# Kernel optimization log

Measured on AMD Instinct MI355X. Metric: run time of the kernel, lower is better.

The kernel has to match this reference:

```python
import jax, jax.numpy as jnp
import numpy as np

N = 50000      # nodes
E = 800000     # edges (before self-loops)
IN = 128       # in_channels
H = 4          # heads
F = 32         # out_channels per head
NEG_SLOPE = 0.2  # GATConv default negative_slope


def setup_inputs() -> dict:
    key = jax.random.key(0)
    k1, k2, k3, k4, k5 = jax.random.split(key, 5)
    x = jax.random.normal(k1, (N, IN), dtype=jnp.float32)
    edge_index = jax.random.randint(k2, (2, E), 0, N, dtype=jnp.int32)
    W = jax.random.normal(k3, (IN, H * F), dtype=jnp.float32) * 0.05
    att_src = jax.random.normal(k4, (H, F), dtype=jnp.float32) * 0.05
    att_dst = jax.random.normal(k5, (H, F), dtype=jnp.float32) * 0.05
    bias = jnp.zeros((H * F,), dtype=jnp.float32)
    return {"x": x, "edge_index": edge_index, "W": W,
            "att_src": att_src, "att_dst": att_dst, "bias": bias}


def reference(x, edge_index, W, att_src, att_dst, bias):
    n = x.shape[0]
    # Linear projection, split into heads: [N, H, F]
    xp = (x @ W).reshape(n, H, F)
    # add_self_loops=True (GATConv default)
    loop = jnp.arange(n, dtype=edge_index.dtype)
    src = jnp.concatenate([edge_index[0], loop])  # [E+N]
    dst = jnp.concatenate([edge_index[1], loop])  # [E+N]
    # Per-node attention logits: [N, H]
    a_s = jnp.einsum('nhf,hf->nh', xp, att_src)
    a_d = jnp.einsum('nhf,hf->nh', xp, att_dst)
    # Edge logits + LeakyReLU: [E+N, H]
    e = jax.nn.leaky_relu(a_s[src] + a_d[dst], NEG_SLOPE)
    # Segment softmax over incoming edges of each dst node
    m = jax.ops.segment_max(e, dst, num_segments=n)  # every node has a self-loop
    e = jnp.exp(e - m[dst])
    denom = jax.ops.segment_sum(e, dst, num_segments=n)
    alpha = e / denom[dst]                     # [E+N, H]
    # Weighted aggregation of source features: [N, H, F]
    msg = alpha[:, :, None] * xp[src]
    out = jax.ops.segment_sum(msg, dst, num_segments=n)
    out = out.reshape(n, H * F) + bias         # concat heads + bias
    return jax.nn.relu(out)                    # wrapper activation (dropout = eval identity)
```

## Files before the change

kernel.cpp:

```cpp
#include <hip/hip_runtime.h>

#define HEADS 4
#define BSHIFT 8

__device__ __forceinline__ unsigned pack_bf16x2(float a, float b) {
  unsigned ua = __builtin_bit_cast(unsigned, a);
  unsigned ub = __builtin_bit_cast(unsigned, b);
  ua = (ua + 0x7FFFu + ((ua >> 16) & 1u)) >> 16;
  ub = (ub + 0x7FFFu + ((ub >> 16) & 1u)) >> 16;
  return ua | (ub << 16);
}
__device__ __forceinline__ float bf_lo(unsigned u) {
  return __builtin_bit_cast(float, u << 16);
}
__device__ __forceinline__ float bf_hi(unsigned u) {
  return __builtin_bit_cast(float, u & 0xFFFF0000u);
}

__global__ __launch_bounds__(256, 4) void k_gemm(
    const float* __restrict__ x, const float* __restrict__ W,
    const float* __restrict__ att_src, const float* __restrict__ att_dst,
    unsigned* __restrict__ xpb, float* __restrict__ a_s, float* __restrict__ a_d, int n)
{
  __shared__ float Wl[32 * 128];
  __shared__ float xs[64 * 36];
  const int tid = threadIdx.x;
  const int row0 = blockIdx.x * 64;
  const int rg = tid & 15;
  const int cg = tid >> 4;

  float acc[4][8];
#pragma unroll
  for (int i = 0; i < 4; ++i)
#pragma unroll
    for (int j = 0; j < 8; ++j) acc[i][j] = 0.f;

  for (int k0 = 0; k0 < 128; k0 += 32) {
    for (int i = tid; i < 1024; i += 256)
      ((float4*)Wl)[i] = ((const float4*)W)[(size_t)k0 * 32 + i];
    for (int i = tid; i < 512; i += 256) {
      const int r = i >> 3, kq = i & 7;
      float4 v = make_float4(0.f, 0.f, 0.f, 0.f);
      if (row0 + r < n) v = ((const float4*)x)[(size_t)(row0 + r) * 32 + (k0 >> 2) + kq];
      *(float4*)&xs[r * 36 + kq * 4] = v;
    }
    __syncthreads();

#pragma unroll
    for (int kk = 0; kk < 32; kk += 4) {
      float4 xr[4];
#pragma unroll
      for (int i = 0; i < 4; ++i) xr[i] = *(const float4*)&xs[(rg + 16 * i) * 36 + kk];
#pragma unroll
      for (int k = 0; k < 4; ++k) {
        float4 w0 = *(const float4*)&Wl[(kk + k) * 128 + 8 * cg];
        float4 w1 = *(const float4*)&Wl[(kk + k) * 128 + 8 * cg + 4];
        const float wv[8] = {w0.x, w0.y, w0.z, w0.w, w1.x, w1.y, w1.z, w1.w};
#pragma unroll
        for (int i = 0; i < 4; ++i) {
          const float xv = (k == 0) ? xr[i].x : (k == 1) ? xr[i].y : (k == 2) ? xr[i].z : xr[i].w;
#pragma unroll
          for (int j = 0; j < 8; ++j) acc[i][j] += xv * wv[j];
        }
      }
    }
    __syncthreads();
  }

  float4 as0 = ((const float4*)att_src)[2 * cg], as1 = ((const float4*)att_src)[2 * cg + 1];
  float4 ad0 = ((const float4*)att_dst)[2 * cg], ad1 = ((const float4*)att_dst)[2 * cg + 1];
  const float asv[8] = {as0.x, as0.y, as0.z, as0.w, as1.x, as1.y, as1.z, as1.w};
  const float adv[8] = {ad0.x, ad0.y, ad0.z, ad0.w, ad1.x, ad1.y, ad1.z, ad1.w};
  const int h = cg >> 2;

#pragma unroll
  for (int i = 0; i < 4; ++i) {
    const int r = row0 + rg + 16 * i;
    if (r < n) {
      uint4 ob;
      ob.x = pack_bf16x2(acc[i][0], acc[i][1]);
      ob.y = pack_bf16x2(acc[i][2], acc[i][3]);
      ob.z = pack_bf16x2(acc[i][4], acc[i][5]);
      ob.w = pack_bf16x2(acc[i][6], acc[i][7]);
      ((uint4*)xpb)[(size_t)r * 16 + cg] = ob;
    }
    float ps = 0.f, pd = 0.f;
#pragma unroll
    for (int j = 0; j < 8; ++j) { ps += acc[i][j] * asv[j]; pd += acc[i][j] * adv[j]; }
    ps += __shfl_xor(ps, 16); pd += __shfl_xor(pd, 16);
    ps += __shfl_xor(ps, 32); pd += __shfl_xor(pd, 32);
    if (r < n && (cg & 3) == 0) {
      a_s[r * HEADS + h] = ps;
      a_d[r * HEADS + h] = pd;
    }
  }
}

__global__ __launch_bounds__(256) void k_hist(
    const int* __restrict__ dst, int* __restrict__ ghist, int E)
{
  __shared__ int h[256];
  const int t = threadIdx.x;
  h[t] = 0;
  __syncthreads();
  int i = blockIdx.x * 1024 + t;
#pragma unroll
  for (int k = 0; k < 4; ++k, i += 256)
    if (i < E) atomicAdd(&h[dst[i] >> BSHIFT], 1);
  __syncthreads();
  if (h[t]) atomicAdd(&ghist[t], h[t]);
}

__global__ __launch_bounds__(256) void k_bscan(
    const int* __restrict__ ghist, int* __restrict__ gstart, int* __restrict__ gcur)
{
  __shared__ int wsum[4];
  const int t = threadIdx.x, lane = t & 63, w = t >> 6;
  const int v = ghist[t];
  int s = v;
#pragma unroll
  for (int o = 1; o < 64; o <<= 1) { int u = __shfl_up(s, o); if (lane >= o) s += u; }
  if (lane == 63) wsum[w] = s;
  __syncthreads();
  int add = 0;
  for (int k = 0; k < w; ++k) add += wsum[k];
  const int excl = add + s - v;
  gstart[t] = excl;
  gcur[t] = excl;
  if (t == 255) gstart[256] = excl + v;
}

__global__ __launch_bounds__(256) void k_part(
    const int* __restrict__ src, const int* __restrict__ dst,
    int* __restrict__ gcur, unsigned* __restrict__ pbuf, int E)
{
  __shared__ unsigned sortbuf[4096];
  __shared__ int hist[256], lstart[256], lcur[256], wbase[256];
  __shared__ int wsum[4];
  const int t = threadIdx.x;
  const int e0 = blockIdx.x * 4096;
  const int cnt = min(4096, E - e0);
  hist[t] = 0;
  __syncthreads();
  for (int i = t; i < cnt; i += 256)
    atomicAdd(&hist[dst[e0 + i] >> BSHIFT], 1);
  __syncthreads();
  const int lane = t & 63, w = t >> 6;
  const int v = hist[t];
  int s = v;
#pragma unroll
  for (int o = 1; o < 64; o <<= 1) { int u = __shfl_up(s, o); if (lane >= o) s += u; }
  if (lane == 63) wsum[w] = s;
  __syncthreads();
  int add = 0;
  for (int k = 0; k < w; ++k) add += wsum[k];
  const int ls = add + s - v;
  lstart[t] = ls;
  lcur[t] = ls;
  wbase[t] = (v > 0) ? atomicAdd(&gcur[t], v) : 0;
  __syncthreads();
  for (int i = t; i < cnt; i += 256) {
    const int d = dst[e0 + i], sE = src[e0 + i];
    const int r = atomicAdd(&lcur[d >> BSHIFT], 1);
    sortbuf[r] = ((unsigned)d << 16) | (unsigned)sE;
  }
  __syncthreads();
  for (int i = t; i < cnt; i += 256) {
    const unsigned p = sortbuf[i];
    const int b = (int)(p >> (16 + BSHIFT));
    pbuf[wbase[b] + (i - lstart[b])] = p;
  }
}

__global__ __launch_bounds__(256) void k_fill2(
    const unsigned* __restrict__ pbuf, const int* __restrict__ gstart,
    int* __restrict__ offs, int* __restrict__ eidx, int n, int E)
{
  __shared__ int cnt[256], base[256];
  __shared__ int wsum[4];
  const int b = blockIdx.x, t = threadIdx.x;
  const int node0 = b << BSHIFT;
  const int ebeg = gstart[b], eend = gstart[b + 1];
  cnt[t] = 0;
  __syncthreads();
  for (int i = ebeg + t; i < eend; i += 256)
    atomicAdd(&cnt[(pbuf[i] >> 16) & 255], 1);
  __syncthreads();
  const int lane = t & 63, w = t >> 6;
  const int v = cnt[t];
  int s = v;
#pragma unroll
  for (int o = 1; o < 64; o <<= 1) { int u = __shfl_up(s, o); if (lane >= o) s += u; }
  if (lane == 63) wsum[w] = s;
  __syncthreads();
  int add = 0;
  for (int k = 0; k < w; ++k) add += wsum[k];
  base[t] = ebeg + add + s - v;
  if (node0 + t < n) offs[node0 + t] = base[t];
  __syncthreads();
  for (int i = ebeg + t; i < eend; i += 256) {
    const unsigned p = pbuf[i];
    const int pos = atomicAdd(&base[(p >> 16) & 255], 1);
    eidx[pos] = (int)(p & 0xFFFFu);
  }
  if (b == 0 && t == 0) offs[n] = E;
}

__global__ __launch_bounds__(256) void k_aggr(
    const unsigned* __restrict__ xpb, const float* __restrict__ a_s,
    const float* __restrict__ a_d, const int* __restrict__ offs,
    const int* __restrict__ eidx, const float* __restrict__ bias,
    float* __restrict__ out, int n)
{
  const int wid = (blockIdx.x * blockDim.x + threadIdx.x) >> 6;
  const int lane = threadIdx.x & 63;
  if (wid >= n) return;
  const int h = lane >> 4;

  const float adh = a_d[wid * HEADS + h];

  float l = a_s[wid * HEADS + h] + adh;
  l = l > 0.f ? l : 0.2f * l;
  const float pself = __expf(l);
  float den = pself;
  const unsigned uself = xpb[(size_t)wid * 64 + lane];
  float accx = pself * bf_lo(uself), accy = pself * bf_hi(uself);

  const int beg = offs[wid], end = offs[wid + 1];
  int e = beg;
  int nb = (end - beg) >> 2;

#define LOADB(s0, s1, s2, s3, u0, u1, u2, u3, b0, b1, b2, b3)            \
  {                                                                      \
    s0 = eidx[e]; s1 = eidx[e + 1]; s2 = eidx[e + 2]; s3 = eidx[e + 3];  \
    u0 = xpb[(size_t)s0 * 64 + lane]; b0 = a_s[s0 * HEADS + h];          \
    u1 = xpb[(size_t)s1 * 64 + lane]; b1 = a_s[s1 * HEADS + h];          \
    u2 = xpb[(size_t)s2 * 64 + lane]; b2 = a_s[s2 * HEADS + h];          \
    u3 = xpb[(size_t)s3 * 64 + lane]; b3 = a_s[s3 * HEADS + h];          \
    e += 4;                                                              \
  }
#define CONSUME(u0, u1, u2, u3, b0, b1, b2, b3)                          \
  {                                                                      \
    float l0 = b0 + adh; l0 = l0 > 0.f ? l0 : 0.2f * l0;                 \
    float l1 = b1 + adh; l1 = l1 > 0.f ? l1 : 0.2f * l1;                 \
    float l2 = b2 + adh; l2 = l2 > 0.f ? l2 : 0.2f * l2;                 \
    float l3 = b3 + adh; l3 = l3 > 0.f ? l3 : 0.2f * l3;                 \
    const float p0 = __expf(l0), p1 = __expf(l1);                        \
    const float p2 = __expf(l2), p3 = __expf(l3);                        \
    den += p0 + p1 + p2 + p3;                                            \
    accx += p0 * bf_lo(u0) + p1 * bf_lo(u1) + p2 * bf_lo(u2) + p3 * bf_lo(u3); \
    accy += p0 * bf_hi(u0) + p1 * bf_hi(u1) + p2 * bf_hi(u2) + p3 * bf_hi(u3); \
  }

  if (nb > 0) {
    int sa0, sa1, sa2, sa3, sb0, sb1, sb2, sb3;
    unsigned ua0, ua1, ua2, ua3, ub0, ub1, ub2, ub3;
    float ba0, ba1, ba2, ba3, bb0, bb1, bb2, bb3;
    LOADB(sa0, sa1, sa2, sa3, ua0, ua1, ua2, ua3, ba0, ba1, ba2, ba3);
    --nb;
    while (nb >= 2) {
      LOADB(sb0, sb1, sb2, sb3, ub0, ub1, ub2, ub3, bb0, bb1, bb2, bb3);
      CONSUME(ua0, ua1, ua2, ua3, ba0, ba1, ba2, ba3);
      LOADB(sa0, sa1, sa2, sa3, ua0, ua1, ua2, ua3, ba0, ba1, ba2, ba3);
      CONSUME(ub0, ub1, ub2, ub3, bb0, bb1, bb2, bb3);
      nb -= 2;
    }
    if (nb == 1) {
      LOADB(sb0, sb1, sb2, sb3, ub0, ub1, ub2, ub3, bb0, bb1, bb2, bb3);
      CONSUME(ua0, ua1, ua2, ua3, ba0, ba1, ba2, ba3);
      CONSUME(ub0, ub1, ub2, ub3, bb0, bb1, bb2, bb3);
    } else {
      CONSUME(ua0, ua1, ua2, ua3, ba0, ba1, ba2, ba3);
    }
  }
  for (; e < end; ++e) {
    const int s = eidx[e];
    const unsigned u = xpb[(size_t)s * 64 + lane];
    float lv = a_s[s * HEADS + h] + adh;
    lv = lv > 0.f ? lv : 0.2f * lv;
    const float p = __expf(lv);
    den += p;
    accx += p * bf_lo(u);
    accy += p * bf_hi(u);
  }
#undef LOADB
#undef CONSUME

  const float2 b2 = ((const float2*)bias)[lane];
  const float inv = 1.f / den;
  float ox = accx * inv + b2.x;
  float oy = accy * inv + b2.y;
  float2 o = make_float2(ox > 0.f ? ox : 0.f, oy > 0.f ? oy : 0.f);
  ((float2*)out)[(size_t)wid * 64 + lane] = o;
}

extern "C" void kernel_launch(void* const* d_in, const int* in_sizes, int n_in,
                              void* d_out, int out_size, void* d_ws, size_t ws_size,
                              hipStream_t stream) {
  const float* x       = (const float*)d_in[0];
  const int*   ei      = (const int*)d_in[1];
  const float* W       = (const float*)d_in[2];
  const float* att_src = (const float*)d_in[3];
  const float* att_dst = (const float*)d_in[4];
  const float* bias    = (const float*)d_in[5];
  float* out = (float*)d_out;
  const int n = in_sizes[0] / 128;
  const int E = in_sizes[1] / 2;
  const int* srce = ei;
  const int* dste = ei + E;

  char* ws = (char*)d_ws;
  size_t o = 0;
  unsigned* xpb = (unsigned*)(ws + o); o += (size_t)n * 128 * 2;
  o = (o + 255) & ~(size_t)255;
  float* a_s = (float*)(ws + o); o += (size_t)n * HEADS * 4;
  float* a_d = (float*)(ws + o); o += (size_t)n * HEADS * 4;
  int* ghist  = (int*)(ws + o);  o += 256 * 4;
  int* gstart = (int*)(ws + o);  o += 260 * 4;
  int* gcur   = (int*)(ws + o);  o += 256 * 4;
  int* offs   = (int*)(ws + o);  o += (size_t)(n + 4) * 4;
  int* eidx   = (int*)(ws + o);  o += (size_t)E * 4;
  unsigned* pbuf = (unsigned*)(ws + o); o += (size_t)E * 4;

  const int NB = (n + 255) >> BSHIFT;
  hipMemsetAsync(ghist, 0, 256 * 4, stream);
  k_hist<<<(E + 1023) / 1024, 256, 0, stream>>>(dste, ghist, E);
  k_bscan<<<1, 256, 0, stream>>>(ghist, gstart, gcur);
  k_part<<<(E + 4095) / 4096, 256, 0, stream>>>(srce, dste, gcur, pbuf, E);
  k_fill2<<<NB, 256, 0, stream>>>(pbuf, gstart, offs, eidx, n, E);
  k_gemm<<<(n + 63) / 64, 256, 0, stream>>>(x, W, att_src, att_dst, xpb, a_s, a_d, n);
  k_aggr<<<(n + 3) / 4, 256, 0, stream>>>(xpb, a_s, a_d, offs, eidx, bias, out, n);
}
```

Before: 130.7 us.

## Use bf16 MFMA for projection GEMM and fold histogram reset into it

Replaces the fp32 FMA register-tiled projection GEMM with a bf16 MFMA 16x16x32 version. Both x and W are converted to bf16 in shared memory, and outputs are staged in LDS for coalesced stores. The attention logits are now computed from the bf16-rounded projections rather than fp32 accumulators, which changes numerics slightly. The GEMM launch moves to the front and zeroes the histogram buffer, removing a separate memset call. Every block still reloads and transposes all of W into LDS, and the larger shared footprint may reduce occupancy.

```diff
diff --git a/kernel.cpp b/kernel.cpp
--- a/kernel.cpp
+++ b/kernel.cpp
@@ -3,12 +3,16 @@
 #define HEADS 4
 #define BSHIFT 8
 
-__device__ __forceinline__ unsigned pack_bf16x2(float a, float b) {
-  unsigned ua = __builtin_bit_cast(unsigned, a);
-  unsigned ub = __builtin_bit_cast(unsigned, b);
-  ua = (ua + 0x7FFFu + ((ua >> 16) & 1u)) >> 16;
-  ub = (ub + 0x7FFFu + ((ub >> 16) & 1u)) >> 16;
-  return ua | (ub << 16);
+typedef __attribute__((ext_vector_type(8))) short bf16x8;
+typedef __attribute__((ext_vector_type(4))) float f32x4;
+
+__device__ __forceinline__ unsigned short f2bf(float f) {
+  unsigned u = __builtin_bit_cast(unsigned, f);
+  u = (u + 0x7FFFu + ((u >> 16) & 1u)) >> 16;
+  return (unsigned short)u;
+}
+__device__ __forceinline__ float bf2f(unsigned short s) {
+  return __builtin_bit_cast(float, (unsigned)s << 16);
 }
 __device__ __forceinline__ float bf_lo(unsigned u) {
   return __builtin_bit_cast(float, u << 16);
@@ -17,82 +21,86 @@
   return __builtin_bit_cast(float, u & 0xFFFF0000u);
 }
 
-__global__ __launch_bounds__(256, 4) void k_gemm(
+__global__ __launch_bounds__(256) void k_gemm(
     const float* __restrict__ x, const float* __restrict__ W,
     const float* __restrict__ att_src, const float* __restrict__ att_dst,
-    unsigned* __restrict__ xpb, float* __restrict__ a_s, float* __restrict__ a_d, int n)
-{
-  __shared__ float Wl[32 * 128];
-  __shared__ float xs[64 * 36];
+    unsigned* __restrict__ xpb, float* __restrict__ a_s, float* __restrict__ a_d,
+    int* __restrict__ ghist, int n)
+{
+  __shared__ unsigned short xb[64 * 136];
+  __shared__ unsigned short Wt[128 * 136];
   const int tid = threadIdx.x;
   const int row0 = blockIdx.x * 64;
-  const int rg = tid & 15;
-  const int cg = tid >> 4;
-
-  float acc[4][8];
-#pragma unroll
-  for (int i = 0; i < 4; ++i)
-#pragma unroll
-    for (int j = 0; j < 8; ++j) acc[i][j] = 0.f;
-
-  for (int k0 = 0; k0 < 128; k0 += 32) {
-    for (int i = tid; i < 1024; i += 256)
-      ((float4*)Wl)[i] = ((const float4*)W)[(size_t)k0 * 32 + i];
-    for (int i = tid; i < 512; i += 256) {
-      const int r = i >> 3, kq = i & 7;
-      float4 v = make_float4(0.f, 0.f, 0.f, 0.f);
-      if (row0 + r < n) v = ((const float4*)x)[(size_t)(row0 + r) * 32 + (k0 >> 2) + kq];
-      *(float4*)&xs[r * 36 + kq * 4] = v;
-    }
-    __syncthreads();
-
-#pragma unroll
-    for (int kk = 0; kk < 32; kk += 4) {
-      float4 xr[4];
-#pragma unroll
-      for (int i = 0; i < 4; ++i) xr[i] = *(const float4*)&xs[(rg + 16 * i) * 36 + kk];
-#pragma unroll
-      for (int k = 0; k < 4; ++k) {
-        float4 w0 = *(const float4*)&Wl[(kk + k) * 128 + 8 * cg];
-        float4 w1 = *(const float4*)&Wl[(kk + k) * 128 + 8 * cg + 4];
-        const float wv[8] = {w0.x, w0.y, w0.z, w0.w, w1.x, w1.y, w1.z, w1.w};
-#pragma unroll
-        for (int i = 0; i < 4; ++i) {
-          const float xv = (k == 0) ? xr[i].x : (k == 1) ? xr[i].y : (k == 2) ? xr[i].z : xr[i].w;
-#pragma unroll
-          for (int j = 0; j < 8; ++j) acc[i][j] += xv * wv[j];
-        }
-      }
-    }
-    __syncthreads();
-  }
-
-  float4 as0 = ((const float4*)att_src)[2 * cg], as1 = ((const float4*)att_src)[2 * cg + 1];
-  float4 ad0 = ((const float4*)att_dst)[2 * cg], ad1 = ((const float4*)att_dst)[2 * cg + 1];
-  const float asv[8] = {as0.x, as0.y, as0.z, as0.w, as1.x, as1.y, as1.z, as1.w};
-  const float adv[8] = {ad0.x, ad0.y, ad0.z, ad0.w, ad1.x, ad1.y, ad1.z, ad1.w};
-  const int h = cg >> 2;
-
-#pragma unroll
-  for (int i = 0; i < 4; ++i) {
-    const int r = row0 + rg + 16 * i;
-    if (r < n) {
-      uint4 ob;
-      ob.x = pack_bf16x2(acc[i][0], acc[i][1]);
-      ob.y = pack_bf16x2(acc[i][2], acc[i][3]);
-      ob.z = pack_bf16x2(acc[i][4], acc[i][5]);
-      ob.w = pack_bf16x2(acc[i][6], acc[i][7]);
-      ((uint4*)xpb)[(size_t)r * 16 + cg] = ob;
-    }
+  if (blockIdx.x == 0) ghist[tid] = 0;
+
+  for (int u = tid; u < 2048; u += 256) {
+    const int r = u >> 5, cq = u & 31;
+    float4 v = make_float4(0.f, 0.f, 0.f, 0.f);
+    if (row0 + r < n) v = ((const float4*)x)[(size_t)(row0 + r) * 32 + cq];
+    unsigned short* p = &xb[r * 136 + cq * 4];
+    p[0] = f2bf(v.x); p[1] = f2bf(v.y); p[2] = f2bf(v.z); p[3] = f2bf(v.w);
+  }
+  for (int u = tid; u < 4096; u += 256) {
+    const int k = u >> 5, cq = u & 31;
+    const float4 v = ((const float4*)W)[u];
+    Wt[(4 * cq + 0) * 136 + k] = f2bf(v.x);
+    Wt[(4 * cq + 1) * 136 + k] = f2bf(v.y);
+    Wt[(4 * cq + 2) * 136 + k] = f2bf(v.z);
+    Wt[(4 * cq + 3) * 136 + k] = f2bf(v.w);
+  }
+  __syncthreads();
+
+  const int wv = tid >> 6;
+  const int lane = tid & 63;
+  const int r = lane & 15, g = lane >> 4;
+
+  f32x4 acc[8];
+#pragma unroll
+  for (int t = 0; t < 8; ++t) acc[t] = (f32x4){0.f, 0.f, 0.f, 0.f};
+
+  bf16x8 afr[4];
+#pragma unroll
+  for (int kc = 0; kc < 4; ++kc)
+    afr[kc] = *(const bf16x8*)&xb[(16 * wv + r) * 136 + kc * 32 + g * 8];
+
+#pragma unroll
+  for (int kc = 0; kc < 4; ++kc) {
+#pragma unroll
+    for (int t = 0; t < 8; ++t) {
+      const bf16x8 bfr = *(const bf16x8*)&Wt[(16 * t + r) * 136 + kc * 32 + g * 8];
+      acc[t] = __builtin_amdgcn_mfma_f32_16x16x32_bf16(afr[kc], bfr, acc[t], 0, 0, 0);
+    }
+  }
+  __syncthreads();
+
+  unsigned short* obuf = Wt;
+#pragma unroll
+  for (int t = 0; t < 8; ++t) {
+#pragma unroll
+    for (int j = 0; j < 4; ++j)
+      obuf[(16 * wv + 4 * g + j) * 132 + 16 * t + r] = f2bf(acc[t][j]);
+  }
+  __syncthreads();
+
+  {
+    const int row = tid >> 2, h = tid & 3;
     float ps = 0.f, pd = 0.f;
-#pragma unroll
-    for (int j = 0; j < 8; ++j) { ps += acc[i][j] * asv[j]; pd += acc[i][j] * adv[j]; }
-    ps += __shfl_xor(ps, 16); pd += __shfl_xor(pd, 16);
-    ps += __shfl_xor(ps, 32); pd += __shfl_xor(pd, 32);
-    if (r < n && (cg & 3) == 0) {
-      a_s[r * HEADS + h] = ps;
-      a_d[r * HEADS + h] = pd;
-    }
+    const unsigned short* orow = &obuf[row * 132 + 32 * h];
+#pragma unroll 8
+    for (int j = 0; j < 32; ++j) {
+      const float v = bf2f(orow[j]);
+      ps += v * att_src[32 * h + j];
+      pd += v * att_dst[32 * h + j];
+    }
+    if (row0 + row < n) {
+      a_s[(row0 + row) * HEADS + h] = ps;
+      a_d[(row0 + row) * HEADS + h] = pd;
+    }
+  }
+  for (int u = tid; u < 2048; u += 256) {
+    const int row = u >> 5, q = u & 31;
+    if (row0 + row < n)
+      ((uint2*)xpb)[(size_t)(row0 + row) * 32 + q] = *(const uint2*)&obuf[row * 132 + q * 4];
   }
 }
 
@@ -323,11 +331,10 @@
   unsigned* pbuf = (unsigned*)(ws + o); o += (size_t)E * 4;
 
   const int NB = (n + 255) >> BSHIFT;
-  hipMemsetAsync(ghist, 0, 256 * 4, stream);
+  k_gemm<<<(n + 63) / 64, 256, 0, stream>>>(x, W, att_src, att_dst, xpb, a_s, a_d, ghist, n);
   k_hist<<<(E + 1023) / 1024, 256, 0, stream>>>(dste, ghist, E);
   k_bscan<<<1, 256, 0, stream>>>(ghist, gstart, gcur);
   k_part<<<(E + 4095) / 4096, 256, 0, stream>>>(srce, dste, gcur, pbuf, E);
   k_fill2<<<NB, 256, 0, stream>>>(pbuf, gstart, offs, eidx, n, E);
-  k_gemm<<<(n + 63) / 64, 256, 0, stream>>>(x, W, att_src, att_dst, xpb, a_s, a_d, n);
   k_aggr<<<(n + 3) / 4, 256, 0, stream>>>(xpb, a_s, a_d, offs, eidx, bias, out, n);
 }
```

Measured after the change: 121.4 us. -7.1%, faster.
